# Performance work log

Measured on AMD Instinct MI355X. Metric: run time of the kernel, lower is better.

Reference implementation:

```python
import jax, jax.numpy as jnp
import numpy as np

B, C, D, H, W = 4, 64, 16, 16, 16
C8 = C // 8


def setup_inputs() -> dict:
    key = jax.random.key(0)
    ks = jax.random.split(key, 9)
    s = lambda k, sh: jax.random.normal(k, sh, dtype=jnp.float32)
    return {
        "x_source": s(ks[0], (B, C, D, H, W)),
        "x_target": s(ks[1], (B, C, D, H, W)),
        "Wq": s(ks[2], (C8, C)) * 0.05,
        "bq": s(ks[3], (C8,)) * 0.05,
        "Wk": s(ks[4], (C8, C)) * 0.05,
        "bk": s(ks[5], (C8,)) * 0.05,
        "Wv": s(ks[6], (C, C)) * 0.05,
        "bv": s(ks[7], (C,)) * 0.05,
        "gamma": s(ks[8], (1,)) * 0.1,
    }


def reference(x_source, x_target, Wq, bq, Wk, bk, Wv, bv, gamma):
    b, c, d, h, w = x_source.shape
    n = d * h * w
    xs = x_source.reshape(b, c, n)   # (B, C, N)
    xt = x_target.reshape(b, c, n)
    # 1x1x1 convs == per-token linear projections
    q = jnp.einsum("oc,bcn->bno", Wq, xt) + bq[None, None, :]   # (B, N, C8)
    k = jnp.einsum("oc,bcn->bon", Wk, xs) + bk[None, :, None]   # (B, C8, N)
    v = jnp.einsum("oc,bcn->bon", Wv, xs) + bv[None, :, None]   # (B, C, N)
    # unscaled single-head full attention over all N = D*H*W tokens
    attn = jax.nn.softmax(jnp.einsum("bno,bom->bnm", q, k), axis=-1)  # (B, N, N)
    out = jnp.einsum("bcm,bnm->bcn", v, attn)                   # (B, C, N)
    out = out.reshape(b, c, d, h, w)
    return gamma * out + x_target
```

## Files before the change

### kernel.cpp

```cpp
#include <hip/hip_runtime.h>
#include <hip/hip_bf16.h>


typedef __attribute__((ext_vector_type(8)))  short s16x8;
typedef __attribute__((ext_vector_type(16))) float f32x16;

constexpr int B  = 4;
constexpr int C  = 64;
constexpr int N  = 4096;
constexpr int CH = 32;
constexpr int NC = 32;

__device__ __forceinline__ ushort f2bf(float x) {
    union { __hip_bfloat16 h; ushort u; } cv;
    cv.h = __float2bfloat16(x);
    return cv.u;
}
__device__ __forceinline__ uint pk2(float a, float b) {
    union { __hip_bfloat162 h2; uint u; } cv;
    cv.h2.x = __float2bfloat16(a);
    cv.h2.y = __float2bfloat16(b);
    return cv.u;
}
__device__ __forceinline__ float exp2_fast(float x) {
#if __has_builtin(__builtin_amdgcn_exp2f)
    return __builtin_amdgcn_exp2f(x);
#else
    float e;
    asm("v_exp_f32 %0, %1" : "=v"(e) : "v"(x));
    return e;
#endif
}

__global__ __launch_bounds__(320) void proj_kernel(
    const float* __restrict__ xs, const float* __restrict__ xt,
    const float* __restrict__ Wq, const float* __restrict__ bq,
    const float* __restrict__ Wk, const float* __restrict__ bk,
    const float* __restrict__ Wv, const float* __restrict__ bv,
    ushort* __restrict__ qg, ushort* __restrict__ kg, ushort* __restrict__ vtg)
{
    const int tid = threadIdx.x;
    const int grp = tid >> 5;
    const int tok = tid & 31;
    const int b   = blockIdx.x >> 7;
    const int n   = ((blockIdx.x & 127) << 5) + tok;

    const float* Wsel; const float* bsel; const float* xsel;
    if (grp < 8)       { Wsel = Wv + grp * 8 * C; bsel = bv + grp * 8; xsel = xs; }
    else if (grp == 8) { Wsel = Wk;               bsel = bk;           xsel = xs; }
    else               { Wsel = Wq;               bsel = bq;           xsel = xt; }

    float acc[8];
#pragma unroll
    for (int j = 0; j < 8; j++) acc[j] = bsel[j];

    const float* xcol = xsel + (size_t)b * C * N + n;
#pragma unroll 2
    for (int ci = 0; ci < C; ci += 4) {
        float x0 = xcol[(size_t)(ci + 0) * N];
        float x1 = xcol[(size_t)(ci + 1) * N];
        float x2 = xcol[(size_t)(ci + 2) * N];
        float x3 = xcol[(size_t)(ci + 3) * N];
#pragma unroll
        for (int j = 0; j < 8; j++) {
            const float4 w4 = *(const float4*)&Wsel[j * C + ci];
            acc[j] += w4.x * x0 + w4.y * x1 + w4.z * x2 + w4.w * x3;
        }
    }

    if (grp < 8) {
#pragma unroll
        for (int j = 0; j < 8; j++)
            vtg[((size_t)b * C + grp * 8 + j) * N + n] = f2bf(acc[j]);
    } else {
        if (grp == 9) {
#pragma unroll
            for (int j = 0; j < 8; j++) acc[j] *= 1.4426950408889634f;
        }
        uint4 wv;
        wv.x = pk2(acc[0], acc[1]); wv.y = pk2(acc[2], acc[3]);
        wv.z = pk2(acc[4], acc[5]); wv.w = pk2(acc[6], acc[7]);
        ushort* dst = (grp == 8 ? kg : qg) + ((size_t)b * N + n) * 8;
        *(uint4*)dst = wv;
    }
}

__global__ __launch_bounds__(512, 2) void attn_kernel(
    const ushort* __restrict__ qg, const ushort* __restrict__ kg,
    const ushort* __restrict__ vtg, const float* __restrict__ xt,
    const float* __restrict__ gamma, float* __restrict__ out)
{
    __shared__ float comb[2][3][64][33];
    __shared__ float combd[2][3][32];

    const int tid  = threadIdx.x;
    const int w    = tid >> 6;
    const int l    = tid & 63;
    const int q32  = l & 31;
    const int G    = l >> 5;
    const bool g1  = (G != 0);

    const int bid  = blockIdx.x;
    const int xcd  = bid & 7;
    const int slot = bid >> 3;
    const int b    = xcd >> 1;
    const int tp   = ((xcd & 1) << 5) | slot;

    const int tile    = w >> 2;
    const int quarter = w & 3;
    const int qbase   = tp * 64 + tile * 32;
    const int kbase   = quarter * 1024;

    const ushort* kgb = kg  + (size_t)b * N * 8;
    const ushort* qgb = qg  + (size_t)b * N * 8;
    const ushort* vgb = vtg + (size_t)b * C * N;

    s16x8 qf;
    {
        const s16x8 z8 = {};
        const s16x8 qv = *(const s16x8*)(qgb + (size_t)(qbase + q32) * 8);
        qf = g1 ? z8 : qv;
    }

    auto kload = [&](int chunk) -> s16x8 {
        return *(const s16x8*)(kgb + (size_t)(kbase + chunk * CH + q32) * 8);
    };
    const ushort* vrow0 = vgb + (size_t)q32 * N + 8 * G;
    const ushort* vrow1 = vgb + (size_t)(q32 + 32) * N + 8 * G;

    f32x16 acc0 = {}; f32x16 acc1 = {};
    float d0 = 0.f, d1 = 0.f, d2 = 0.f, d3 = 0.f;

    s16x8 kcur = kload(0);
    s16x8 va0, va1, va2, va3;
    {
        va0 = *(const s16x8*)(vrow0 + kbase);
        va1 = *(const s16x8*)(vrow1 + kbase);
        va2 = *(const s16x8*)(vrow0 + kbase + 16);
        va3 = *(const s16x8*)(vrow1 + kbase + 16);
    }

#pragma unroll 2
    for (int c0 = 0; c0 < NC; ++c0) {
        const int cn  = (c0 + 1 < NC) ? c0 + 1 : c0;
        const int kof = kbase + cn * CH;
        const s16x8 knx = kload(cn);
        const s16x8 vb0 = *(const s16x8*)(vrow0 + kof);
        const s16x8 vb1 = *(const s16x8*)(vrow1 + kof);
        const s16x8 vb2 = *(const s16x8*)(vrow0 + kof + 16);
        const s16x8 vb3 = *(const s16x8*)(vrow1 + kof + 16);

        __builtin_amdgcn_s_barrier();

        f32x16 sf = {};
        sf = __builtin_amdgcn_mfma_f32_32x32x16_bf16(kcur, qf, sf, 0, 0, 0);

        float p[16];
#pragma unroll
        for (int r = 0; r < 16; r++) p[r] = exp2_fast(sf[r]);
#pragma unroll
        for (int r = 0; r < 16; r += 4) {
            d0 += p[r]; d1 += p[r + 1]; d2 += p[r + 2]; d3 += p[r + 3];
        }

#pragma unroll
        for (int ks = 0; ks < 2; ++ks) {
            uint wd[4];
#pragma unroll
            for (int i = 0; i < 2; i++) {
                const int base = 2 * i + 8 * ks;
                const uint XO = pk2(p[base + 0], p[base + 1]);
                const uint XH = pk2(p[base + 4], p[base + 5]);
                const uint Y  = g1 ? XO : XH;
                const uint Z  = (uint)__shfl_xor((int)Y, 32);
                wd[0 + i] = g1 ? Z : XO;
                wd[2 + i] = g1 ? XH : Z;
            }
            union { uint u[4]; s16x8 v; } bu;
            bu.u[0] = wd[0]; bu.u[1] = wd[1]; bu.u[2] = wd[2]; bu.u[3] = wd[3];

            const s16x8 a0 = ks ? va2 : va0;
            const s16x8 a1 = ks ? va3 : va1;
            acc0 = __builtin_amdgcn_mfma_f32_32x32x16_bf16(a0, bu.v, acc0, 0, 0, 0);
            acc1 = __builtin_amdgcn_mfma_f32_32x32x16_bf16(a1, bu.v, acc1, 0, 0, 0);
        }

        kcur = knx;
        va0 = vb0; va1 = vb1; va2 = vb2; va3 = vb3;
    }

    float dsum = (d0 + d1) + (d2 + d3);
    dsum += __shfl_xor(dsum, 32);

    if (quarter != 0) {
        float* row = &comb[tile][quarter - 1][l][0];
#pragma unroll
        for (int e = 0; e < 16; e++) row[e]      = acc0[e];
#pragma unroll
        for (int e = 0; e < 16; e++) row[16 + e] = acc1[e];
        if (l < 32) combd[tile][quarter - 1][l] = dsum;
    }
    __syncthreads();
    if (quarter == 0) {
        const float g    = gamma[0];
        const float dtot = dsum + combd[tile][0][q32]
                                + combd[tile][1][q32]
                                + combd[tile][2][q32];
        const float inv  = 1.0f / dtot;
        const float* r0  = &comb[tile][0][l][0];
        const float* r1  = &comb[tile][1][l][0];
        const float* r2  = &comb[tile][2][l][0];
#pragma unroll
        for (int r = 0; r < 16; r++) {
            const int crow = (r & 3) + 8 * (r >> 2) + 4 * G;
            const size_t a0 = ((size_t)b * C + crow) * N + qbase + q32;
            const size_t a1 = ((size_t)b * C + crow + 32) * N + qbase + q32;
            const float o0 = (acc0[r] + r0[r]      + r1[r]      + r2[r])      * inv;
            const float o1 = (acc1[r] + r0[16 + r] + r1[16 + r] + r2[16 + r]) * inv;
            out[a0] = g * o0 + xt[a0];
            out[a1] = g * o1 + xt[a1];
        }
    }
}

extern "C" void kernel_launch(void* const* d_in, const int* in_sizes, int n_in,
                              void* d_out, int out_size, void* d_ws, size_t ws_size,
                              hipStream_t stream) {
    const float* xs    = (const float*)d_in[0];
    const float* xt    = (const float*)d_in[1];
    const float* Wq    = (const float*)d_in[2];
    const float* bq    = (const float*)d_in[3];
    const float* Wk    = (const float*)d_in[4];
    const float* bk    = (const float*)d_in[5];
    const float* Wv    = (const float*)d_in[6];
    const float* bv    = (const float*)d_in[7];
    const float* gamma = (const float*)d_in[8];
    float* out = (float*)d_out;

    ushort* qg  = (ushort*)d_ws;
    ushort* kg  = qg + (size_t)B * N * 8;
    ushort* vtg = kg + (size_t)B * N * 8;

    proj_kernel<<<(B * N) / 32, 320, 0, stream>>>(xs, xt, Wq, bq, Wk, bk, Wv, bv,
                                                  qg, kg, vtg);
    attn_kernel<<<B * 64, 512, 0, stream>>>(qg, kg, vtg, xt, gamma, out);
}
```

Before: 128.6 us.

## Store V in MFMA-fragment layout and stage projection weights in LDS

The projection kernel now writes V in a pre-swizzled layout matching the MFMA A-operand fragment order, so each lane in the attention kernel reads contiguous 16-byte chunks with fully coalesced wave-wide loads instead of strided row accesses. The projection kernel also copies the weights and biases into shared memory once per block, replacing repeated global loads. The trade-off is scattered 2-byte stores in the projection kernel and a block-wide synchronisation at its start.

After: 114.0 us. -11.4%, faster.

```diff
diff --git a/kernel.cpp b/kernel.cpp
--- a/kernel.cpp
+++ b/kernel.cpp
@@ -37,18 +37,30 @@
     const float* __restrict__ Wq, const float* __restrict__ bq,
     const float* __restrict__ Wk, const float* __restrict__ bk,
     const float* __restrict__ Wv, const float* __restrict__ bv,
-    ushort* __restrict__ qg, ushort* __restrict__ kg, ushort* __restrict__ vtg)
+    ushort* __restrict__ qg, ushort* __restrict__ kg, ushort* __restrict__ vf)
 {
+    __shared__ float sWv[64 * 64];
+    __shared__ float sWk[8 * 64];
+    __shared__ float sWq[8 * 64];
+    __shared__ float sB[80];
+
     const int tid = threadIdx.x;
+    for (int i = tid; i < 4096; i += 320) sWv[i] = Wv[i];
+    for (int i = tid; i < 512;  i += 320) { sWk[i] = Wk[i]; sWq[i] = Wq[i]; }
+    if (tid < 64)                sB[tid] = bv[tid];
+    else if (tid < 72)           sB[tid] = bk[tid - 64];
+    else if (tid < 80)           sB[tid] = bq[tid - 72];
+    __syncthreads();
+
     const int grp = tid >> 5;
     const int tok = tid & 31;
     const int b   = blockIdx.x >> 7;
     const int n   = ((blockIdx.x & 127) << 5) + tok;
 
     const float* Wsel; const float* bsel; const float* xsel;
-    if (grp < 8)       { Wsel = Wv + grp * 8 * C; bsel = bv + grp * 8; xsel = xs; }
-    else if (grp == 8) { Wsel = Wk;               bsel = bk;           xsel = xs; }
-    else               { Wsel = Wq;               bsel = bq;           xsel = xt; }
+    if (grp < 8)       { Wsel = sWv + grp * 8 * C; bsel = sB + grp * 8; xsel = xs; }
+    else if (grp == 8) { Wsel = sWk;               bsel = sB + 64;      xsel = xs; }
+    else               { Wsel = sWq;               bsel = sB + 72;      xsel = xt; }
 
     float acc[8];
 #pragma unroll
@@ -69,9 +81,17 @@
     }
 
     if (grp < 8) {
-#pragma unroll
-        for (int j = 0; j < 8; j++)
-            vtg[((size_t)b * C + grp * 8 + j) * N + n] = f2bf(acc[j]);
+        const int c   = n >> 5;
+        const int kk  = n & 31;
+        const int ks  = kk >> 4;
+        const int Gd  = (kk >> 3) & 1;
+        const int j   = kk & 7;
+        const int f   = grp >> 2;
+        const int cb  = (grp & 3) * 8;
+        ushort* base = vf + ((size_t)(b * 128 + c) * 2048) + ks * 1024 + f * 512 + j;
+#pragma unroll
+        for (int jc = 0; jc < 8; jc++)
+            base[(size_t)(Gd * 32 + cb + jc) * 8] = f2bf(acc[jc]);
     } else {
         if (grp == 9) {
 #pragma unroll
@@ -87,7 +107,7 @@
 
 __global__ __launch_bounds__(512, 2) void attn_kernel(
     const ushort* __restrict__ qg, const ushort* __restrict__ kg,
-    const ushort* __restrict__ vtg, const float* __restrict__ xt,
+    const ushort* __restrict__ vf, const float* __restrict__ xt,
     const float* __restrict__ gamma, float* __restrict__ out)
 {
     __shared__ float comb[2][3][64][33];
@@ -110,10 +130,11 @@
     const int quarter = w & 3;
     const int qbase   = tp * 64 + tile * 32;
     const int kbase   = quarter * 1024;
-
-    const ushort* kgb = kg  + (size_t)b * N * 8;
-    const ushort* qgb = qg  + (size_t)b * N * 8;
-    const ushort* vgb = vtg + (size_t)b * C * N;
+    const int cbase   = quarter * 32;
+
+    const ushort* kgb = kg + (size_t)b * N * 8;
+    const ushort* qgb = qg + (size_t)b * N * 8;
+    const ushort* vfb = vf + (size_t)b * 128 * 2048;
 
     s16x8 qf;
     {
@@ -125,8 +146,7 @@
     auto kload = [&](int chunk) -> s16x8 {
         return *(const s16x8*)(kgb + (size_t)(kbase + chunk * CH + q32) * 8);
     };
-    const ushort* vrow0 = vgb + (size_t)q32 * N + 8 * G;
-    const ushort* vrow1 = vgb + (size_t)(q32 + 32) * N + 8 * G;
+    const ushort* vl = vfb + (size_t)l * 8;
 
     f32x16 acc0 = {}; f32x16 acc1 = {};
     float d0 = 0.f, d1 = 0.f, d2 = 0.f, d3 = 0.f;
@@ -134,21 +154,22 @@
     s16x8 kcur = kload(0);
     s16x8 va0, va1, va2, va3;
     {
-        va0 = *(const s16x8*)(vrow0 + kbase);
-        va1 = *(const s16x8*)(vrow1 + kbase);
-        va2 = *(const s16x8*)(vrow0 + kbase + 16);
-        va3 = *(const s16x8*)(vrow1 + kbase + 16);
+        const ushort* vc = vl + (size_t)cbase * 2048;
+        va0 = *(const s16x8*)(vc + 0);
+        va1 = *(const s16x8*)(vc + 512);
+        va2 = *(const s16x8*)(vc + 1024);
+        va3 = *(const s16x8*)(vc + 1536);
     }
 
 #pragma unroll 2
     for (int c0 = 0; c0 < NC; ++c0) {
         const int cn  = (c0 + 1 < NC) ? c0 + 1 : c0;
-        const int kof = kbase + cn * CH;
         const s16x8 knx = kload(cn);
-        const s16x8 vb0 = *(const s16x8*)(vrow0 + kof);
-        const s16x8 vb1 = *(const s16x8*)(vrow1 + kof);
-        const s16x8 vb2 = *(const s16x8*)(vrow0 + kof + 16);
-        const s16x8 vb3 = *(const s16x8*)(vrow1 + kof + 16);
+        const ushort* vc = vl + (size_t)(cbase + cn) * 2048;
+        const s16x8 vb0 = *(const s16x8*)(vc + 0);
+        const s16x8 vb1 = *(const s16x8*)(vc + 512);
+        const s16x8 vb2 = *(const s16x8*)(vc + 1024);
+        const s16x8 vb3 = *(const s16x8*)(vc + 1536);
 
         __builtin_amdgcn_s_barrier();
 
@@ -237,11 +258,11 @@
     const float* gamma = (const float*)d_in[8];
     float* out = (float*)d_out;
 
-    ushort* qg  = (ushort*)d_ws;
-    ushort* kg  = qg + (size_t)B * N * 8;
-    ushort* vtg = kg + (size_t)B * N * 8;
+    ushort* qg = (ushort*)d_ws;
+    ushort* kg = qg + (size_t)B * N * 8;
+    ushort* vfp = kg + (size_t)B * N * 8;
 
     proj_kernel<<<(B * N) / 32, 320, 0, stream>>>(xs, xt, Wq, bq, Wk, bk, Wv, bv,
-                                                  qg, kg, vtg);
-    attn_kernel<<<B * 64, 512, 0, stream>>>(qg, kg, vtg, xt, gamma, out);
-}
+                                                  qg, kg, vfp);
+    attn_kernel<<<B * 64, 512, 0, stream>>>(qg, kg, vfp, xt, gamma, out);
+}
```
